# Kernel optimization log

Measured on AMD Instinct MI355X. Metric: run time of the kernel, lower is better.

The kernel has to match this reference:

```python
import jax, jax.numpy as jnp
import numpy as np

E_DIM = 1024   # encoder output dim
H = 320        # prediction-net hidden size
V = 29         # vocab incl. blank
BLANK = 28     # blank index (last)
SOS = -1       # start-of-sequence sentinel
JH = 512       # joint hidden
MAX_SYM = 3    # max symbols per time step
B, T, F_IN = 16, 128, 240


def lstm_step(x, h, c, Wih, Whh, bih, bhh):
    # torch LSTMCell gate order: i, f, g, o
    gates = x @ Wih.T + h @ Whh.T + bih + bhh
    i, f, g, o = jnp.split(gates, 4, axis=-1)
    i = jax.nn.sigmoid(i); f = jax.nn.sigmoid(f)
    g = jnp.tanh(g); o = jax.nn.sigmoid(o)
    c2 = f * c + i * g
    return o * jnp.tanh(c2), c2


def greedy_decode(feats, out_lens, embed, Wih0, Whh0, bih0, bhh0,
                  Wih1, Whh1, bih1, bhh1, Wj1, bj1, Wj2, bj2):
    # feats: [B, T, E_DIM]; returns padded labels [B, T*MAX_SYM] (pad=-1) and counts [B]
    Tn = feats.shape[1]
    buf = Tn * MAX_SYM

    def one(f_seq, L):
        def tstep(carry, inp):
            f, t = inp

            def body(_, st):
                h, c, last, labels, count, nb = st
                active = nb & (t < L)
                # prediction step: SOS -> zero embedding; hidden starts as zeros (== None)
                adj = jnp.where(last > BLANK, last - 1, last)
                e = jnp.where(last == SOS, 0.0, 1.0) * embed[jnp.clip(adj, 0, V - 2)]
                h0, c0 = lstm_step(e, h[0], c[0], Wih0, Whh0, bih0, bhh0)
                h1, c1 = lstm_step(h0, h[1], c[1], Wih1, Whh1, bih1, bhh1)
                # joint step (no log-normalize, matching log_normalize=False)
                logits = jax.nn.relu(jnp.concatenate([f, h1]) @ Wj1 + bj1) @ Wj2 + bj2
                k = jnp.argmax(logits).astype(jnp.int32)
                is_blank = k == BLANK
                emit = active & (~is_blank)
                labels = labels.at[count].set(jnp.where(emit, k, labels[count]))
                count = count + emit.astype(jnp.int32)
                last = jnp.where(emit, k, last)
                # hidden only advances on non-blank emission (as in the torch loop)
                h = jnp.where(emit, jnp.stack([h0, h1]), h)
                c = jnp.where(emit, jnp.stack([c0, c1]), c)
                nb = nb & (~is_blank)
                return (h, c, last, labels, count, nb)

            h, c, last, labels, count = carry
            h, c, last, labels, count, _ = jax.lax.fori_loop(
                0, MAX_SYM, body, (h, c, last, labels, count, jnp.array(True)))
            return (h, c, last, labels, count), None

        init = (jnp.zeros((2, H), feats.dtype), jnp.zeros((2, H), feats.dtype),
                jnp.int32(SOS), jnp.full((buf,), -1, jnp.int32), jnp.int32(0))
        (h, c, last, labels, count), _ = jax.lax.scan(
            tstep, init, (f_seq, jnp.arange(Tn)))
        return labels, count

    return jax.vmap(one)(feats, out_lens)


def setup_inputs() -> dict:
    key = jax.random.key(0)
    ks = jax.random.split(key, 16)
    s = 0.1
    n = lambda k, sh: jax.random.normal(k, sh, jnp.float32) * s
    return {
        "x": jax.random.normal(ks[0], (B, T, F_IN), jnp.float32),
        "out_lens": jax.random.randint(ks[1], (B,), 1, T + 1, dtype=jnp.int32),
        "W_enc": n(ks[2], (F_IN, E_DIM)), "b_enc": jnp.zeros((E_DIM,), jnp.float32),
        "embed": n(ks[3], (V - 1, H)),
        "Wih0": n(ks[4], (4 * H, H)), "Whh0": n(ks[5], (4 * H, H)),
        "bih0": jnp.zeros((4 * H,), jnp.float32), "bhh0": jnp.zeros((4 * H,), jnp.float32),
        "Wih1": n(ks[6], (4 * H, H)), "Whh1": n(ks[7], (4 * H, H)),
        "bih1": jnp.zeros((4 * H,), jnp.float32), "bhh1": jnp.zeros((4 * H,), jnp.float32),
        "Wj1": n(ks[8], (E_DIM + H, JH)), "bj1": jnp.zeros((JH,), jnp.float32),
        "Wj2": n(ks[9], (JH, V)), "bj2": jnp.zeros((V,), jnp.float32),
    }


def reference(x, out_lens, W_enc, b_enc, embed, Wih0, Whh0, bih0, bhh0,
              Wih1, Whh1, bih1, bhh1, Wj1, bj1, Wj2, bj2):
    # encoder (stand-in for model.encoder): linear projection, T preserved
    logits = x @ W_enc + b_enc  # [B, T, E_DIM]
    labels, counts = greedy_decode(logits, out_lens, embed,
                                   Wih0, Whh0, bih0, bhh0,
                                   Wih1, Whh1, bih1, bhh1,
                                   Wj1, bj1, Wj2, bj2)
    return logits, out_lens, labels, counts
```

## Files before the change

### kernel.cpp

```cpp
#include <hip/hip_runtime.h>
#include <math.h>

#define BB 16
#define TT 128
#define F_IN 240
#define E_DIM 1024
#define HH 320
#define G4 1280
#define JHD 512
#define VV 29
#define BLANKV 28
#define MAXSYM 3
#define LBUF (TT*MAXSYM)

#define GROUPS 8
#define RPG 20
#define NBLK (GROUPS*RPG)
#define HR 16
#define JR 32
#define CROLES 16

#define OFF_FPROJ 0ul
#define OFF_WJHR  1048576ul
#define OFF_EP    (OFF_WJHR + 163840ul)
#define OFF_B1    (OFF_EP + 37120ul)
#define OFF_WJ2T  (OFF_B1 + 1280ul)
#define OFF_MA    (OFF_WJ2T + 14848ul)
#define OFF_MB    (OFF_MA + 5120ul)
#define OFF_JH    (OFF_MB + 5120ul)
#define OFF_SYNC  (OFF_JH + 8192ul)

typedef float f32x4 __attribute__((ext_vector_type(4)));

__device__ __forceinline__ float sigmoidf_(float x) {
    return 1.0f / (1.0f + expf(-x));
}
__device__ __forceinline__ int ld_tag(const int* p) {
    return __hip_atomic_load(p, __ATOMIC_RELAXED, __HIP_MEMORY_SCOPE_AGENT);
}
__device__ __forceinline__ void st_tag(int* p, int v) {
    __hip_atomic_store(p, v, __ATOMIC_RELAXED, __HIP_MEMORY_SCOPE_AGENT);
}
__device__ __forceinline__ void st_data_f(float* p, float v, int pure) {
    if (pure) asm volatile("global_store_dword %0, %1, off sc0" :: "v"(p), "v"(v) : "memory");
    else      asm volatile("global_store_dword %0, %1, off sc0 sc1" :: "v"(p), "v"(v) : "memory");
}
__device__ __forceinline__ f32x4 ld4_data(const float* p, int pure) {
    f32x4 v;
    if (pure) asm volatile("global_load_dwordx4 %0, %1, off sc0\n\ts_waitcnt vmcnt(0)"
                           : "=&v"(v) : "v"(p) : "memory");
    else      asm volatile("global_load_dwordx4 %0, %1, off sc0 sc1\n\ts_waitcnt vmcnt(0)"
                           : "=&v"(v) : "v"(p) : "memory");
    return v;
}

__global__ void prep_t_kernel(const float* __restrict__ Wj1,
                              const float* __restrict__ bih1,
                              const float* __restrict__ bhh1,
                              const float* __restrict__ Wj2,
                              float* __restrict__ WjhR, float* __restrict__ b1,
                              float* __restrict__ Wj2T) {
    int idx = blockIdx.x * 256 + threadIdx.x;
    if (idx < 163840) {
        int j = idx / 320, k = idx - j * 320;
        WjhR[idx] = Wj1[(size_t)(1024 + k) * JHD + j];
        return;
    }
    int i2 = idx - 163840;
    if (i2 < G4) { b1[i2] = bih1[i2] + bhh1[i2]; return; }
    int e = i2 - G4;
    if (e < VV * JHD) {
        int v = e >> 9, k = e & 511;
        Wj2T[e] = Wj2[(size_t)k * VV + v];
    }
}

__global__ void ep_kernel(const float* __restrict__ embed,
                          const float* __restrict__ Wih0,
                          const float* __restrict__ bih0,
                          const float* __restrict__ bhh0,
                          float* __restrict__ EP) {
    __shared__ __align__(16) float es[HH];
    int v = blockIdx.x;
    for (int k = threadIdx.x; k < HH; k += 256)
        es[k] = (v < VV - 1) ? embed[v * HH + k] : 0.0f;
    __syncthreads();
    for (int j = threadIdx.x; j < G4; j += 256) {
        float acc = bih0[j] + bhh0[j];
        if (v < VV - 1) {
            const float4* wr = (const float4*)(Wih0 + (size_t)j * HH);
            const float4* ev = (const float4*)es;
            #pragma unroll 4
            for (int k4 = 0; k4 < HH / 4; ++k4) {
                float4 w = wr[k4], e = ev[k4];
                acc += w.x * e.x + w.y * e.y + w.z * e.z + w.w * e.w;
            }
        }
        EP[v * G4 + j] = acc;
    }
}

__global__ __launch_bounds__(512) void enc_fproj_kernel(
    const float* __restrict__ x, const float* __restrict__ Wenc,
    const float* __restrict__ benc, const float* __restrict__ Wj1,
    const float* __restrict__ bj1,
    float* __restrict__ logits_out, float* __restrict__ Fproj) {
    __shared__ float xs[8][F_IN];
    __shared__ float ls[8][E_DIM];
    int row0 = blockIdx.x * 8;
    int tid = threadIdx.x;
    for (int i = tid; i < 8 * F_IN; i += 512)
        xs[i / F_IN][i % F_IN] = x[(size_t)row0 * F_IN + i];
    __syncthreads();
    for (int j = tid; j < E_DIM; j += 512) {
        float acc[8];
        float bv = benc[j];
        #pragma unroll
        for (int r = 0; r < 8; ++r) acc[r] = bv;
        for (int k = 0; k < F_IN; ++k) {
            float w = Wenc[(size_t)k * E_DIM + j];
            #pragma unroll
            for (int r = 0; r < 8; ++r) acc[r] += xs[r][k] * w;
        }
        #pragma unroll
        for (int r = 0; r < 8; ++r) {
            ls[r][j] = acc[r];
            logits_out[(size_t)(row0 + r) * E_DIM + j] = acc[r];
        }
    }
    __syncthreads();
    {
        int j = tid;
        float acc[8];
        float bv = bj1[j];
        #pragma unroll
        for (int r = 0; r < 8; ++r) acc[r] = bv;
        for (int k = 0; k < E_DIM; ++k) {
            float w = Wj1[(size_t)k * JHD + j];
            #pragma unroll
            for (int r = 0; r < 8; ++r) acc[r] += ls[r][k] * w;
        }
        #pragma unroll
        for (int r = 0; r < 8; ++r) Fproj[(size_t)(row0 + r) * JHD + j] = acc[r];
    }
}

__global__ void init_kernel(const int* __restrict__ lens, float* ws,
                            float* __restrict__ out_lens_out,
                            float* __restrict__ labels_out) {
    int tid = threadIdx.x;
    int* sync = (int*)(ws + OFF_SYNC);
    for (int i = tid; i < 2048; i += 1024) sync[i] = 0;
    for (int i = tid; i < BB * LBUF; i += 1024) labels_out[i] = -1.0f;
    if (tid < BB) out_lens_out[tid] = (float)lens[tid];
}

__global__ __launch_bounds__(1024) void decode_persistent(
    const int* __restrict__ lens,
    const float* __restrict__ Fproj,
    const float* __restrict__ W0,
    const float* __restrict__ W1a,
    const float* __restrict__ W1b,
    const float* __restrict__ WjhR,
    const float* __restrict__ Wj2T,
    const float* __restrict__ EP, const float* __restrict__ b1,
    const float* __restrict__ bj2,
    float* MA, float* MB, float* JH, int* syncw,
    float* __restrict__ labels_out, float* __restrict__ counts_out) {

    const int tid = threadIdx.x;
    int* cntw = syncw;
    int* arrw = syncw + 128;
    int* tags = syncw + 256;

    __shared__ int sGrp, sRole, sPure;
    if (tid == 0) {
        unsigned xr;
        asm volatile("s_getreg_b32 %0, hwreg(HW_REG_XCC_ID)" : "=s"(xr));
        int xcc = (int)(xr & 7u);
        int tkt = atomicAdd(cntw + xcc * 16, 1);
        asm volatile("s_waitcnt vmcnt(0)" ::: "memory");
        atomicAdd(arrw, 1);
        while (__hip_atomic_load(arrw, __ATOMIC_RELAXED, __HIP_MEMORY_SCOPE_AGENT) < NBLK) { }
        int c[8];
        #pragma unroll
        for (int h = 0; h < 8; ++h)
            c[h] = __hip_atomic_load(cntw + h * 16, __ATOMIC_RELAXED,
                                     __HIP_MEMORY_SCOPE_AGENT);
        int grp, role;
        if (tkt < RPG) { grp = xcc; role = tkt; }
        else {
            int ov = tkt - RPG;
            for (int h = 0; h < xcc; ++h) ov += max(0, c[h] - RPG);
            grp = -1; role = 0;
            int acc = 0;
            for (int g2 = 0; g2 < 8; ++g2) {
                int granted = min(c[g2], RPG);
                int d = RPG - granted;
                if (grp < 0 && ov < acc + d) { grp = g2; role = granted + (ov - acc); }
                acc += d;
            }
        }
        sGrp = grp; sRole = role;
        sPure = (c[grp] >= RPG) ? 1 : 0;
    }
    __syncthreads();
    const int grp = sGrp, role = sRole, pure = sPure;

    float* MAg = MA + grp * 640;
    float* MBg = MB + grp * 640;
    float* JHg = JH + grp * 1024;
    int* tagA = tags + grp * 96;
    int* tagB = tagA + 32;
    int* tagC = tagA + 64;

    extern __shared__ float dyn[];
    float* h0c = dyn;
    float* h1c = dyn + 640;
    float* h0p = dyn + 1280;
    float* h1p = dyn + 1920;
    float* jhl = dyn + 2560;

    __shared__ float gA[128], gB[128], lgL[64];
    __shared__ int lastL[2], cntL[2], contL[2], lenL[2], emitL[2];

    for (int i = tid; i < 640; i += 1024) { h0c[i] = 0.f; h1c[i] = 0.f; }
    if (tid < 2) {
        lastL[tid] = BLANKV; cntL[tid] = 0; contL[tid] = 0;
        lenL[tid] = lens[2 * grp + tid];
    }
    __syncthreads();
    const int maxL = max(lenL[0], lenL[1]);

    const int item = tid & 1;
    const int ks   = (tid >> 1) & 7;
    const int r    = tid >> 4;
    const int gg   = r >> 4, rl = r & 15;
    const int hrow = role * HR + rl;
    const int kf   = ks * 40;
    const size_t wrow = (size_t)(gg * HH + hrow) * HH + kf;

    float c0cur = 0.f, c1cur = 0.f, c0p = 0.f, c1p = 0.f;

    for (int slot = 0; slot < 3 * maxL; ++slot) {
        const int t = slot / 3;
        const int s = slot - t * 3;
        const int e = slot + 1;

        {
            float a0 = 0.f, ab = 0.f;
            const f32x4* h0 = (const f32x4*)(h0c + item * HH + kf);
            const f32x4* h1 = (const f32x4*)(h1c + item * HH + kf);
            #pragma unroll
            for (int u = 0; u < 10; ++u) {
                f32x4 w  = *(const f32x4*)(W0 + wrow + u * 4);
                f32x4 h  = h0[u];
                a0 += w[0]*h[0] + w[1]*h[1] + w[2]*h[2] + w[3]*h[3];
                f32x4 w2 = *(const f32x4*)(W1b + wrow + u * 4);
                f32x4 h2 = h1[u];
                ab += w2[0]*h2[0] + w2[1]*h2[1] + w2[2]*h2[2] + w2[3]*h2[3];
            }
            a0 += __shfl_xor(a0, 2); a0 += __shfl_xor(a0, 4); a0 += __shfl_xor(a0, 8);
            ab += __shfl_xor(ab, 2); ab += __shfl_xor(ab, 4); ab += __shfl_xor(ab, 8);
            if (ks == 0) {
                gA[item * 64 + r] = a0 + EP[(size_t)lastL[item] * G4 + gg * HH + hrow];
                gB[item * 64 + r] = ab;
            }
        }
        __syncthreads();
        if (tid < 32) {
            int it = tid & 1, hr = tid >> 1;
            float xi = gA[it * 64 + hr];
            float xf = gA[it * 64 + 16 + hr];
            float xg = gA[it * 64 + 32 + hr];
            float xo = gA[it * 64 + 48 + hr];
            c0p = sigmoidf_(xf) * c0cur + sigmoidf_(xi) * tanhf(xg);
            st_data_f(MAg + it * HH + role * HR + hr, sigmoidf_(xo) * tanhf(c0p), pure);
        }
        asm volatile("s_waitcnt vmcnt(0)" ::: "memory");
        __syncthreads();
        if (tid == 0) st_tag(tagA + role, e);

        if (tid < 64) {
            while (__ballot((tid < RPG) && (ld_tag(tagA + tid) < e)) != 0ull) { }
        }
        __syncthreads();
        if (tid < 160) {
            f32x4 v = ld4_data(MAg + tid * 4, pure);
            int it = tid / 80, k = tid * 4 - it * 320;
            *(f32x4*)(h0p + it * HH + k) = v;
        }
        __syncthreads();

        {
            float a1 = 0.f;
            const f32x4* hv = (const f32x4*)(h0p + item * HH + kf);
            #pragma unroll
            for (int u = 0; u < 10; ++u) {
                f32x4 w = *(const f32x4*)(W1a + wrow + u * 4);
                f32x4 h = hv[u];
                a1 += w[0]*h[0] + w[1]*h[1] + w[2]*h[2] + w[3]*h[3];
            }
            a1 += __shfl_xor(a1, 2); a1 += __shfl_xor(a1, 4); a1 += __shfl_xor(a1, 8);
            if (ks == 0)
                gA[item * 64 + r] = a1 + gB[item * 64 + r] + b1[gg * HH + hrow];
        }
        __syncthreads();
        if (tid < 32) {
            int it = tid & 1, hr = tid >> 1;
            float xi = gA[it * 64 + hr];
            float xf = gA[it * 64 + 16 + hr];
            float xg = gA[it * 64 + 32 + hr];
            float xo = gA[it * 64 + 48 + hr];
            c1p = sigmoidf_(xf) * c1cur + sigmoidf_(xi) * tanhf(xg);
            st_data_f(MBg + it * HH + role * HR + hr, sigmoidf_(xo) * tanhf(c1p), pure);
        }
        asm volatile("s_waitcnt vmcnt(0)" ::: "memory");
        __syncthreads();
        if (tid == 0) st_tag(tagB + role, e);

        if (tid < 64) {
            while (__ballot((tid < RPG) && (ld_tag(tagB + tid) < e)) != 0ull) { }
        }
        __syncthreads();
        if (tid < 160) {
            f32x4 v = ld4_data(MBg + tid * 4, pure);
            int it = tid / 80, k = tid * 4 - it * 320;
            *(f32x4*)(h1p + it * HH + k) = v;
        }
        __syncthreads();

        if (role < CROLES && tid < 512) {
            int jl = tid >> 4;
            int jg2 = role * JR + jl;
            float a = 0.f;
            const f32x4* hv = (const f32x4*)(h1p + item * HH + kf);
            const float* wc = WjhR + (size_t)jg2 * HH + kf;
            #pragma unroll
            for (int u = 0; u < 10; ++u) {
                f32x4 w = *(const f32x4*)(wc + u * 4);
                f32x4 h = hv[u];
                a += w[0]*h[0] + w[1]*h[1] + w[2]*h[2] + w[3]*h[3];
            }
            a += __shfl_xor(a, 2); a += __shfl_xor(a, 4); a += __shfl_xor(a, 8);
            if (ks == 0) {
                float fp = Fproj[((size_t)(2 * grp + item) * TT + t) * JHD + jg2];
                st_data_f(JHg + item * JHD + jg2, fmaxf(a + fp, 0.f), pure);
            }
        }
        asm volatile("s_waitcnt vmcnt(0)" ::: "memory");
        __syncthreads();
        if (role < CROLES && tid == 0) st_tag(tagC + role, e);

        if (tid < 64) {
            while (__ballot((tid < CROLES) && (ld_tag(tagC + tid) < e)) != 0ull) { }
        }
        __syncthreads();
        if (tid < 256) {
            f32x4 v = ld4_data(JHg + tid * 4, pure);
            int it = tid / 128, k = tid * 4 - it * 512;
            *(f32x4*)(jhl + it * JHD + k) = v;
        }
        __syncthreads();

        if (tid < 928) {
            int k4 = tid & 15, it2 = (tid >> 4) & 1, v = tid >> 5;
            const float* wv = Wj2T + (size_t)v * JHD + k4 * 32;
            const f32x4* hj = (const f32x4*)(jhl + it2 * JHD + k4 * 32);
            float a = 0.f;
            #pragma unroll
            for (int u2 = 0; u2 < 8; ++u2) {
                f32x4 w = *(const f32x4*)(wv + u2 * 4);
                f32x4 h = hj[u2];
                a += w[0]*h[0] + w[1]*h[1] + w[2]*h[2] + w[3]*h[3];
            }
            a += __shfl_xor(a, 1); a += __shfl_xor(a, 2);
            a += __shfl_xor(a, 4); a += __shfl_xor(a, 8);
            if (k4 == 0) lgL[it2 * 32 + v] = a + bj2[v];
        }
        __syncthreads();
        if (tid < 2) {
            float best = lgL[tid * 32];
            int k = 0;
            #pragma unroll
            for (int v = 1; v < VV; ++v) {
                float x = lgL[tid * 32 + v];
                if (x > best) { best = x; k = v; }
            }
            bool active = (t < lenL[tid]) && (s == 0 || contL[tid]);
            bool emit = active && (k != BLANKV);
            emitL[tid] = emit ? 1 : 0;
            if (emit) {
                if (role == 0)
                    labels_out[(size_t)(2 * grp + tid) * LBUF + cntL[tid]] = (float)k;
                cntL[tid]++; lastL[tid] = k; contL[tid] = 1;
            } else {
                contL[tid] = 0;
            }
        }
        __syncthreads();
        if (tid < 640) {
            int it = tid / 320, k = tid - it * 320;
            if (emitL[it]) {
                h0c[it * HH + k] = h0p[it * HH + k];
                h1c[it * HH + k] = h1p[it * HH + k];
            }
        }
        if (tid < 32 && emitL[tid & 1]) { c0cur = c0p; c1cur = c1p; }
        __syncthreads();
    }

    if (role == 0 && tid < 2) counts_out[2 * grp + tid] = (float)cntL[tid];
}

extern "C" void kernel_launch(void* const* d_in, const int* in_sizes, int n_in,
                              void* d_out, int out_size, void* d_ws, size_t ws_size,
                              hipStream_t stream) {
    const float* x      = (const float*)d_in[0];
    const int*   lens   = (const int*)d_in[1];
    const float* Wenc   = (const float*)d_in[2];
    const float* benc   = (const float*)d_in[3];
    const float* embed  = (const float*)d_in[4];
    const float* Wih0   = (const float*)d_in[5];
    const float* Whh0   = (const float*)d_in[6];
    const float* bih0   = (const float*)d_in[7];
    const float* bhh0   = (const float*)d_in[8];
    const float* Wih1   = (const float*)d_in[9];
    const float* Whh1   = (const float*)d_in[10];
    const float* bih1   = (const float*)d_in[11];
    const float* bhh1   = (const float*)d_in[12];
    const float* Wj1    = (const float*)d_in[13];
    const float* bj1    = (const float*)d_in[14];
    const float* Wj2    = (const float*)d_in[15];
    const float* bj2    = (const float*)d_in[16];

    float* out = (float*)d_out;
    float* logits_out   = out;
    float* out_lens_out = out + (size_t)BB * TT * E_DIM;
    float* labels_out   = out_lens_out + BB;
    float* counts_out   = labels_out + (size_t)BB * LBUF;

    float* ws    = (float*)d_ws;
    float* Fproj = ws + OFF_FPROJ;
    float* WjhR  = ws + OFF_WJHR;
    float* EP    = ws + OFF_EP;
    float* b1    = ws + OFF_B1;
    float* Wj2T  = ws + OFF_WJ2T;
    float* MA    = ws + OFF_MA;
    float* MB    = ws + OFF_MB;
    float* JH    = ws + OFF_JH;
    int*   syncw = (int*)(ws + OFF_SYNC);

    const int dynBytes = 84 * 1024;
    hipFuncSetAttribute((const void*)decode_persistent,
                        hipFuncAttributeMaxDynamicSharedMemorySize, dynBytes);

    {
        int total = 163840 + G4 + VV * JHD;
        prep_t_kernel<<<(total + 255) / 256, 256, 0, stream>>>(
            Wj1, bih1, bhh1, Wj2, WjhR, b1, Wj2T);
    }
    ep_kernel<<<VV, 256, 0, stream>>>(embed, Wih0, bih0, bhh0, EP);
    enc_fproj_kernel<<<(BB * TT) / 8, 512, 0, stream>>>(x, Wenc, benc, Wj1, bj1,
                                                        logits_out, Fproj);
    init_kernel<<<1, 1024, 0, stream>>>(lens, ws, out_lens_out, labels_out);
    decode_persistent<<<NBLK, 1024, dynBytes, stream>>>(
        lens, Fproj, Whh0, Wih1, Whh1, WjhR, Wj2T, EP, b1, bj2,
        MA, MB, JH, syncw, labels_out, counts_out);
}
```

Before: 10.36 ms.

## Launch one block per CU and poll L2-local fast tags with slow fallback

Launches 256 blocks instead of 160 so every XCC can fill its group of 20 roles from local CUs. Surplus blocks exit early. Inter-block tag polling now reads sc0 (XCC-local L2) copies of the tags, and only every 256 iterations falls back to reading the device-coherent copy. The aim is to cut cross-XCC synchronization latency on each LSTM and joint step. The cost is a double tag store, and for non-pure groups whose tags arrive only via the slow path the polling may add latency.

```diff
diff --git a/kernel.cpp b/kernel.cpp
--- a/kernel.cpp
+++ b/kernel.cpp
@@ -15,7 +15,7 @@
 
 #define GROUPS 8
 #define RPG 20
-#define NBLK (GROUPS*RPG)
+#define NLAUNCH 256
 #define HR 16
 #define JR 32
 #define CROLES 16
@@ -41,6 +41,15 @@
 __device__ __forceinline__ void st_tag(int* p, int v) {
     __hip_atomic_store(p, v, __ATOMIC_RELAXED, __HIP_MEMORY_SCOPE_AGENT);
 }
+__device__ __forceinline__ int ld_sc0_i(const int* p) {
+    int v;
+    asm volatile("global_load_dword %0, %1, off sc0\n\ts_waitcnt vmcnt(0)"
+                 : "=v"(v) : "v"(p) : "memory");
+    return v;
+}
+__device__ __forceinline__ void st_sc0_i(int* p, int v) {
+    asm volatile("global_store_dword %0, %1, off sc0" :: "v"(p), "v"(v) : "memory");
+}
 __device__ __forceinline__ void st_data_f(float* p, float v, int pure) {
     if (pure) asm volatile("global_store_dword %0, %1, off sc0" :: "v"(p), "v"(v) : "memory");
     else      asm volatile("global_store_dword %0, %1, off sc0 sc1" :: "v"(p), "v"(v) : "memory");
@@ -52,6 +61,19 @@
     else      asm volatile("global_load_dwordx4 %0, %1, off sc0 sc1\n\ts_waitcnt vmcnt(0)"
                            : "=&v"(v) : "v"(p) : "memory");
     return v;
+}
+__device__ __forceinline__ void poll_tags(const int* fastT, const int* slowT,
+                                          int n, int e) {
+    int lane = threadIdx.x;
+    int it = 0;
+    while (true) {
+        bool ny = (lane < n) && (ld_sc0_i(fastT + lane) < e);
+        if (__ballot(ny) == 0ull) return;
+        if (((++it) & 255) == 0) {
+            bool ny2 = (lane < n) && (ld_tag(slowT + lane) < e);
+            if (__ballot(ny2) == 0ull) return;
+        }
+    }
 }
 
 __global__ void prep_t_kernel(const float* __restrict__ Wj1,
@@ -169,9 +191,10 @@
     float* __restrict__ labels_out, float* __restrict__ counts_out) {
 
     const int tid = threadIdx.x;
-    int* cntw = syncw;
-    int* arrw = syncw + 128;
-    int* tags = syncw + 256;
+    int* cntw  = syncw;
+    int* arrw  = syncw + 128;
+    int* tagsF = syncw + 256;
+    int* tagsS = syncw + 1024;
 
     __shared__ int sGrp, sRole, sPure;
     if (tid == 0) {
@@ -181,18 +204,17 @@
         int tkt = atomicAdd(cntw + xcc * 16, 1);
         asm volatile("s_waitcnt vmcnt(0)" ::: "memory");
         atomicAdd(arrw, 1);
-        while (__hip_atomic_load(arrw, __ATOMIC_RELAXED, __HIP_MEMORY_SCOPE_AGENT) < NBLK) { }
+        while (__hip_atomic_load(arrw, __ATOMIC_RELAXED, __HIP_MEMORY_SCOPE_AGENT) < NLAUNCH) { }
         int c[8];
         #pragma unroll
         for (int h = 0; h < 8; ++h)
             c[h] = __hip_atomic_load(cntw + h * 16, __ATOMIC_RELAXED,
                                      __HIP_MEMORY_SCOPE_AGENT);
-        int grp, role;
+        int grp = -1, role = 0;
         if (tkt < RPG) { grp = xcc; role = tkt; }
         else {
             int ov = tkt - RPG;
             for (int h = 0; h < xcc; ++h) ov += max(0, c[h] - RPG);
-            grp = -1; role = 0;
             int acc = 0;
             for (int g2 = 0; g2 < 8; ++g2) {
                 int granted = min(c[g2], RPG);
@@ -202,17 +224,18 @@
             }
         }
         sGrp = grp; sRole = role;
-        sPure = (c[grp] >= RPG) ? 1 : 0;
+        sPure = (grp >= 0 && c[grp] >= RPG) ? 1 : 0;
     }
     __syncthreads();
     const int grp = sGrp, role = sRole, pure = sPure;
+    if (grp < 0) return;
 
     float* MAg = MA + grp * 640;
     float* MBg = MB + grp * 640;
     float* JHg = JH + grp * 1024;
-    int* tagA = tags + grp * 96;
-    int* tagB = tagA + 32;
-    int* tagC = tagA + 64;
+    int* fA = tagsF + grp * 96;   int* sA = tagsS + grp * 96;
+    int* fB = fA + 32;            int* sB = sA + 32;
+    int* fC = fA + 64;            int* sC = sA + 64;
 
     extern __shared__ float dyn[];
     float* h0c = dyn;
@@ -279,11 +302,9 @@
         }
         asm volatile("s_waitcnt vmcnt(0)" ::: "memory");
         __syncthreads();
-        if (tid == 0) st_tag(tagA + role, e);
-
-        if (tid < 64) {
-            while (__ballot((tid < RPG) && (ld_tag(tagA + tid) < e)) != 0ull) { }
-        }
+        if (tid == 0) { st_sc0_i(fA + role, e); st_tag(sA + role, e); }
+
+        if (tid < 64) poll_tags(fA, sA, RPG, e);
         __syncthreads();
         if (tid < 160) {
             f32x4 v = ld4_data(MAg + tid * 4, pure);
@@ -317,11 +338,9 @@
         }
         asm volatile("s_waitcnt vmcnt(0)" ::: "memory");
         __syncthreads();
-        if (tid == 0) st_tag(tagB + role, e);
-
-        if (tid < 64) {
-            while (__ballot((tid < RPG) && (ld_tag(tagB + tid) < e)) != 0ull) { }
-        }
+        if (tid == 0) { st_sc0_i(fB + role, e); st_tag(sB + role, e); }
+
+        if (tid < 64) poll_tags(fB, sB, RPG, e);
         __syncthreads();
         if (tid < 160) {
             f32x4 v = ld4_data(MBg + tid * 4, pure);
@@ -350,11 +369,9 @@
         }
         asm volatile("s_waitcnt vmcnt(0)" ::: "memory");
         __syncthreads();
-        if (role < CROLES && tid == 0) st_tag(tagC + role, e);
-
-        if (tid < 64) {
-            while (__ballot((tid < CROLES) && (ld_tag(tagC + tid) < e)) != 0ull) { }
-        }
+        if (role < CROLES && tid == 0) { st_sc0_i(fC + role, e); st_tag(sC + role, e); }
+
+        if (tid < 64) poll_tags(fC, sC, CROLES, e);
         __syncthreads();
         if (tid < 256) {
             f32x4 v = ld4_data(JHg + tid * 4, pure);
@@ -464,7 +481,7 @@
     enc_fproj_kernel<<<(BB * TT) / 8, 512, 0, stream>>>(x, Wenc, benc, Wj1, bj1,
                                                         logits_out, Fproj);
     init_kernel<<<1, 1024, 0, stream>>>(lens, ws, out_lens_out, labels_out);
-    decode_persistent<<<NBLK, 1024, dynBytes, stream>>>(
+    decode_persistent<<<NLAUNCH, 1024, dynBytes, stream>>>(
         lens, Fproj, Whh0, Wih1, Whh1, WjhR, Wj2T, EP, b1, bj2,
         MA, MB, JH, syncw, labels_out, counts_out);
 }
```

New measurement: 41.38 ms. 299% more time.

## Spread LSTM rows over 32 roles per group and cache W0/W1a slices in LDS

Applied to the files above, without the earlier changes.

Each group now has 32 cooperating blocks instead of 20, so each block handles 10 hidden rows per gate instead of 16, and the joint layer uses 16 columns per role. Because each block's slice is smaller, the Whh0 and Wih1 slices are copied once into shared memory and reused every step instead of being re-read from global memory. 256 blocks are launched and surplus blocks exit after group assignment. The change also adds cache writeback and invalidate around ticket assignment. The cost is more blocks joining each cross-block tag barrier, a larger LDS footprint, and the assumption that all 256 blocks are co-resident.

```diff
diff --git a/kernel.cpp b/kernel.cpp
--- a/kernel.cpp
+++ b/kernel.cpp
@@ -14,11 +14,11 @@
 #define LBUF (TT*MAXSYM)
 
 #define GROUPS 8
-#define RPG 20
-#define NBLK (GROUPS*RPG)
-#define HR 16
-#define JR 32
-#define CROLES 16
+#define RPG 32
+#define NLAUNCH 256
+#define HRR 10
+#define JRR 16
+#define WP 324
 
 #define OFF_FPROJ 0ul
 #define OFF_WJHR  1048576ul
@@ -52,6 +52,10 @@
     else      asm volatile("global_load_dwordx4 %0, %1, off sc0 sc1\n\ts_waitcnt vmcnt(0)"
                            : "=&v"(v) : "v"(p) : "memory");
     return v;
+}
+__device__ __forceinline__ void poll_tags(const int* tagp, int n, int e) {
+    int lane = threadIdx.x;
+    while (__ballot((lane < n) && (ld_tag(tagp + lane) < e)) != 0ull) { }
 }
 
 __global__ void prep_t_kernel(const float* __restrict__ Wj1,
@@ -150,7 +154,8 @@
                             float* __restrict__ labels_out) {
     int tid = threadIdx.x;
     int* sync = (int*)(ws + OFF_SYNC);
-    for (int i = tid; i < 2048; i += 1024) sync[i] = 0;
+    for (int i = tid; i < 2048; i += 1024)
+        __hip_atomic_store(sync + i, 0, __ATOMIC_RELAXED, __HIP_MEMORY_SCOPE_AGENT);
     for (int i = tid; i < BB * LBUF; i += 1024) labels_out[i] = -1.0f;
     if (tid < BB) out_lens_out[tid] = (float)lens[tid];
 }
@@ -169,9 +174,9 @@
     float* __restrict__ labels_out, float* __restrict__ counts_out) {
 
     const int tid = threadIdx.x;
-    int* cntw = syncw;
-    int* arrw = syncw + 128;
-    int* tags = syncw + 256;
+    int* cntw  = syncw;
+    int* arrw  = syncw + 128;
+    int* tags  = syncw + 256;
 
     __shared__ int sGrp, sRole, sPure;
     if (tid == 0) {
@@ -179,20 +184,22 @@
         asm volatile("s_getreg_b32 %0, hwreg(HW_REG_XCC_ID)" : "=s"(xr));
         int xcc = (int)(xr & 7u);
         int tkt = atomicAdd(cntw + xcc * 16, 1);
+        asm volatile("buffer_wbl2 sc1" ::: "memory");
+        asm volatile("s_waitcnt vmcnt(0)" ::: "memory");
+        asm volatile("buffer_inv sc0 sc1" ::: "memory");
         asm volatile("s_waitcnt vmcnt(0)" ::: "memory");
         atomicAdd(arrw, 1);
-        while (__hip_atomic_load(arrw, __ATOMIC_RELAXED, __HIP_MEMORY_SCOPE_AGENT) < NBLK) { }
+        while (__hip_atomic_load(arrw, __ATOMIC_RELAXED, __HIP_MEMORY_SCOPE_AGENT) < NLAUNCH) { }
         int c[8];
         #pragma unroll
         for (int h = 0; h < 8; ++h)
             c[h] = __hip_atomic_load(cntw + h * 16, __ATOMIC_RELAXED,
                                      __HIP_MEMORY_SCOPE_AGENT);
-        int grp, role;
+        int grp = -1, role = 0;
         if (tkt < RPG) { grp = xcc; role = tkt; }
         else {
             int ov = tkt - RPG;
             for (int h = 0; h < xcc; ++h) ov += max(0, c[h] - RPG);
-            grp = -1; role = 0;
             int acc = 0;
             for (int g2 = 0; g2 < 8; ++g2) {
                 int granted = min(c[g2], RPG);
@@ -202,10 +209,11 @@
             }
         }
         sGrp = grp; sRole = role;
-        sPure = (c[grp] >= RPG) ? 1 : 0;
+        sPure = (grp >= 0 && c[grp] >= RPG) ? 1 : 0;
     }
     __syncthreads();
     const int grp = sGrp, role = sRole, pure = sPure;
+    if (grp < 0) return;
 
     float* MAg = MA + grp * 640;
     float* MBg = MB + grp * 640;
@@ -215,15 +223,24 @@
     int* tagC = tagA + 64;
 
     extern __shared__ float dyn[];
-    float* h0c = dyn;
-    float* h1c = dyn + 640;
-    float* h0p = dyn + 1280;
-    float* h1p = dyn + 1920;
-    float* jhl = dyn + 2560;
-
-    __shared__ float gA[128], gB[128], lgL[64];
+    float* W0L  = dyn;
+    float* W1aL = dyn + 40 * WP;
+    float* h0c  = dyn + 80 * WP;
+    float* h1c  = h0c + 640;
+    float* h0p  = h1c + 640;
+    float* h1p  = h0p + 640;
+    float* jhl  = h1p + 640;
+
+    __shared__ float gA[80], gB[80], lgL[64];
     __shared__ int lastL[2], cntL[2], contL[2], lenL[2], emitL[2];
 
+    for (int idx = tid; idx < 40 * 320; idx += 1024) {
+        int rr = idx / 320, k = idx - rr * 320;
+        int ggp = rr / HRR, rlp = rr - ggp * HRR;
+        size_t grow = (size_t)(ggp * HH + role * HRR + rlp) * HH + k;
+        W0L[rr * WP + k]  = W0[grow];
+        W1aL[rr * WP + k] = W1a[grow];
+    }
     for (int i = tid; i < 640; i += 1024) { h0c[i] = 0.f; h1c[i] = 0.f; }
     if (tid < 2) {
         lastL[tid] = BLANKV; cntL[tid] = 0; contL[tid] = 0;
@@ -235,10 +252,14 @@
     const int item = tid & 1;
     const int ks   = (tid >> 1) & 7;
     const int r    = tid >> 4;
-    const int gg   = r >> 4, rl = r & 15;
-    const int hrow = role * HR + rl;
+    const bool mv  = (r < 40);
+    const int gg   = r / HRR, rl = r - gg * HRR;
+    const int hrow = role * HRR + rl;
     const int kf   = ks * 40;
     const size_t wrow = (size_t)(gg * HH + hrow) * HH + kf;
+    const int lrow = r * WP + kf;
+
+    const int jlC = tid >> 4;
 
     float c0cur = 0.f, c1cur = 0.f, c0p = 0.f, c1p = 0.f;
 
@@ -247,14 +268,15 @@
         const int s = slot - t * 3;
         const int e = slot + 1;
 
-        {
+        if (mv) {
             float a0 = 0.f, ab = 0.f;
             const f32x4* h0 = (const f32x4*)(h0c + item * HH + kf);
             const f32x4* h1 = (const f32x4*)(h1c + item * HH + kf);
+            const f32x4* w0l = (const f32x4*)(W0L + lrow);
             #pragma unroll
             for (int u = 0; u < 10; ++u) {
-                f32x4 w  = *(const f32x4*)(W0 + wrow + u * 4);
-                f32x4 h  = h0[u];
+                f32x4 w = w0l[u];
+                f32x4 h = h0[u];
                 a0 += w[0]*h[0] + w[1]*h[1] + w[2]*h[2] + w[3]*h[3];
                 f32x4 w2 = *(const f32x4*)(W1b + wrow + u * 4);
                 f32x4 h2 = h1[u];
@@ -263,27 +285,25 @@
             a0 += __shfl_xor(a0, 2); a0 += __shfl_xor(a0, 4); a0 += __shfl_xor(a0, 8);
             ab += __shfl_xor(ab, 2); ab += __shfl_xor(ab, 4); ab += __shfl_xor(ab, 8);
             if (ks == 0) {
-                gA[item * 64 + r] = a0 + EP[(size_t)lastL[item] * G4 + gg * HH + hrow];
-                gB[item * 64 + r] = ab;
-            }
-        }
-        __syncthreads();
-        if (tid < 32) {
+                gA[item * 40 + r] = a0 + EP[(size_t)lastL[item] * G4 + gg * HH + hrow];
+                gB[item * 40 + r] = ab;
+            }
+        }
+        __syncthreads();
+        if (tid < 20) {
             int it = tid & 1, hr = tid >> 1;
-            float xi = gA[it * 64 + hr];
-            float xf = gA[it * 64 + 16 + hr];
-            float xg = gA[it * 64 + 32 + hr];
-            float xo = gA[it * 64 + 48 + hr];
+            float xi = gA[it * 40 + hr];
+            float xf = gA[it * 40 + 10 + hr];
+            float xg = gA[it * 40 + 20 + hr];
+            float xo = gA[it * 40 + 30 + hr];
             c0p = sigmoidf_(xf) * c0cur + sigmoidf_(xi) * tanhf(xg);
-            st_data_f(MAg + it * HH + role * HR + hr, sigmoidf_(xo) * tanhf(c0p), pure);
+            st_data_f(MAg + it * HH + role * HRR + hr, sigmoidf_(xo) * tanhf(c0p), pure);
         }
         asm volatile("s_waitcnt vmcnt(0)" ::: "memory");
         __syncthreads();
         if (tid == 0) st_tag(tagA + role, e);
 
-        if (tid < 64) {
-            while (__ballot((tid < RPG) && (ld_tag(tagA + tid) < e)) != 0ull) { }
-        }
+        if (tid < 64) poll_tags(tagA, RPG, e);
         __syncthreads();
         if (tid < 160) {
             f32x4 v = ld4_data(MAg + tid * 4, pure);
@@ -292,36 +312,35 @@
         }
         __syncthreads();
 
-        {
+        if (mv) {
             float a1 = 0.f;
             const f32x4* hv = (const f32x4*)(h0p + item * HH + kf);
+            const f32x4* w1l = (const f32x4*)(W1aL + lrow);
             #pragma unroll
             for (int u = 0; u < 10; ++u) {
-                f32x4 w = *(const f32x4*)(W1a + wrow + u * 4);
+                f32x4 w = w1l[u];
                 f32x4 h = hv[u];
                 a1 += w[0]*h[0] + w[1]*h[1] + w[2]*h[2] + w[3]*h[3];
             }
             a1 += __shfl_xor(a1, 2); a1 += __shfl_xor(a1, 4); a1 += __shfl_xor(a1, 8);
             if (ks == 0)
-                gA[item * 64 + r] = a1 + gB[item * 64 + r] + b1[gg * HH + hrow];
-        }
-        __syncthreads();
-        if (tid < 32) {
+                gA[item * 40 + r] = a1 + gB[item * 40 + r] + b1[gg * HH + hrow];
+        }
+        __syncthreads();
+        if (tid < 20) {
             int it = tid & 1, hr = tid >> 1;
-            float xi = gA[it * 64 + hr];
-            float xf = gA[it * 64 + 16 + hr];
-            float xg = gA[it * 64 + 32 + hr];
-            float xo = gA[it * 64 + 48 + hr];
+            float xi = gA[it * 40 + hr];
+            float xf = gA[it * 40 + 10 + hr];
+            float xg = gA[it * 40 + 20 + hr];
+            float xo = gA[it * 40 + 30 + hr];
             c1p = sigmoidf_(xf) * c1cur + sigmoidf_(xi) * tanhf(xg);
-            st_data_f(MBg + it * HH + role * HR + hr, sigmoidf_(xo) * tanhf(c1p), pure);
+            st_data_f(MBg + it * HH + role * HRR + hr, sigmoidf_(xo) * tanhf(c1p), pure);
         }
         asm volatile("s_waitcnt vmcnt(0)" ::: "memory");
         __syncthreads();
         if (tid == 0) st_tag(tagB + role, e);
 
-        if (tid < 64) {
-            while (__ballot((tid < RPG) && (ld_tag(tagB + tid) < e)) != 0ull) { }
-        }
+        if (tid < 64) poll_tags(tagB, RPG, e);
         __syncthreads();
         if (tid < 160) {
             f32x4 v = ld4_data(MBg + tid * 4, pure);
@@ -330,9 +349,8 @@
         }
         __syncthreads();
 
-        if (role < CROLES && tid < 512) {
-            int jl = tid >> 4;
-            int jg2 = role * JR + jl;
+        if (tid < 256) {
+            int jg2 = role * JRR + jlC;
             float a = 0.f;
             const f32x4* hv = (const f32x4*)(h1p + item * HH + kf);
             const float* wc = WjhR + (size_t)jg2 * HH + kf;
@@ -350,11 +368,9 @@
         }
         asm volatile("s_waitcnt vmcnt(0)" ::: "memory");
         __syncthreads();
-        if (role < CROLES && tid == 0) st_tag(tagC + role, e);
-
-        if (tid < 64) {
-            while (__ballot((tid < CROLES) && (ld_tag(tagC + tid) < e)) != 0ull) { }
-        }
+        if (tid == 0) st_tag(tagC + role, e);
+
+        if (tid < 64) poll_tags(tagC, RPG, e);
         __syncthreads();
         if (tid < 256) {
             f32x4 v = ld4_data(JHg + tid * 4, pure);
@@ -406,7 +422,7 @@
                 h1c[it * HH + k] = h1p[it * HH + k];
             }
         }
-        if (tid < 32 && emitL[tid & 1]) { c0cur = c0p; c1cur = c1p; }
+        if (tid < 20 && emitL[tid & 1]) { c0cur = c0p; c1cur = c1p; }
         __syncthreads();
     }
 
@@ -451,7 +467,7 @@
     float* JH    = ws + OFF_JH;
     int*   syncw = (int*)(ws + OFF_SYNC);
 
-    const int dynBytes = 84 * 1024;
+    const int dynBytes = (80 * WP + 4 * 640 + 2 * JHD) * 4;
     hipFuncSetAttribute((const void*)decode_persistent,
                         hipFuncAttributeMaxDynamicSharedMemorySize, dynBytes);
 
@@ -464,7 +480,7 @@
     enc_fproj_kernel<<<(BB * TT) / 8, 512, 0, stream>>>(x, Wenc, benc, Wj1, bj1,
                                                         logits_out, Fproj);
     init_kernel<<<1, 1024, 0, stream>>>(lens, ws, out_lens_out, labels_out);
-    decode_persistent<<<NBLK, 1024, dynBytes, stream>>>(
+    decode_persistent<<<NLAUNCH, 1024, dynBytes, stream>>>(
         lens, Fproj, Whh0, Wih1, Whh1, WjhR, Wj2T, EP, b1, bj2,
         MA, MB, JH, syncw, labels_out, counts_out);
 }
```

After: 8.310 ms. -19.8%, faster.
